# Optimization experiments

Measured on AMD Instinct MI355X. Metric: run time of the kernel, lower is better.

Reference implementation:

```python
import jax, jax.numpy as jnp
import numpy as np

N_NODES = 100000
N_EDGES = 600000
D = 128
N_CLASSES = 16


def _degrees(idx, n):
    ones = jnp.ones(idx.shape[0], dtype=jnp.float32)
    return jax.ops.segment_sum(ones, idx, num_segments=n)


def graph_conv(src, dst, h, W, b):
    # DGL GraphConv, norm='both': D_out^{-1/2} A D_in^{-1/2} h W + b
    n = h.shape[0]
    deg_out = jnp.maximum(_degrees(src, n), 1.0)
    deg_in = jnp.maximum(_degrees(dst, n), 1.0)
    h = h * jax.lax.rsqrt(deg_out)[:, None]          # src-side norm
    h = h @ W                                         # dense transform
    msg = h[src]                                      # gather  [E, d]
    agg = jax.ops.segment_sum(msg, dst, num_segments=n)  # scatter-add
    agg = agg * jax.lax.rsqrt(deg_in)[:, None]        # dst-side norm
    return agg + b


def setup_inputs() -> dict:
    key = jax.random.key(0)
    ks = jax.random.split(key, 8)
    h = jax.random.normal(ks[0], (N_NODES, D), dtype=jnp.float32)
    src = jax.random.randint(ks[1], (N_EDGES,), 0, N_NODES)
    dst = jax.random.randint(ks[2], (N_EDGES,), 0, N_NODES)
    s = 1.0 / np.sqrt(D)
    W1 = jax.random.normal(ks[3], (D, D), dtype=jnp.float32) * s
    b1 = jnp.zeros((D,), dtype=jnp.float32)
    W2 = jax.random.normal(ks[4], (D, D), dtype=jnp.float32) * s
    b2 = jnp.zeros((D,), dtype=jnp.float32)
    Wc = jax.random.normal(ks[5], (D, N_CLASSES), dtype=jnp.float32) * s
    bc = jnp.zeros((N_CLASSES,), dtype=jnp.float32)
    return {"h": h, "src": src, "dst": dst, "W1": W1, "b1": b1,
            "W2": W2, "b2": b2, "Wc": Wc, "bc": bc}


def reference(h, src, dst, W1, b1, W2, b2, Wc, bc):
    h = jax.nn.relu(graph_conv(src, dst, h, W1, b1))
    h = jax.nn.relu(graph_conv(src, dst, h, W2, b2))
    return h @ Wc + bc
```

## Files before the change

### kernel.cpp

```cpp
#include <hip/hip_runtime.h>


typedef __attribute__((ext_vector_type(4))) _Float16 half4_t;
typedef __attribute__((ext_vector_type(16))) float floatx16;

__global__ __launch_bounds__(256) void scan1_kernel(
    const int* __restrict__ cntI, const int* __restrict__ cntO,
    int* __restrict__ excl, int* __restrict__ bsum,
    float* __restrict__ rs_out, float* __restrict__ rs_in, int n)
{
    __shared__ int tmp[256];
    int i = blockIdx.x * 256 + threadIdx.x;
    int v = 0;
    if (i < n) {
        v = cntI[i];
        rs_in[i]  = rsqrtf(fmaxf((float)v, 1.0f));
        rs_out[i] = rsqrtf(fmaxf((float)cntO[i], 1.0f));
    }
    tmp[threadIdx.x] = v;
    __syncthreads();
    for (int off = 1; off < 256; off <<= 1) {
        int t = (threadIdx.x >= off) ? tmp[threadIdx.x - off] : 0;
        __syncthreads();
        tmp[threadIdx.x] += t;
        __syncthreads();
    }
    if (i < n) excl[i] = tmp[threadIdx.x] - v;
    if (threadIdx.x == 255) bsum[blockIdx.x] = tmp[255];
}

__global__ __launch_bounds__(1024) void scan2_kernel(int* __restrict__ bsum, int nb)
{
    __shared__ int tmp[1024];
    int t = threadIdx.x;
    int v = (t < nb) ? bsum[t] : 0;
    tmp[t] = v;
    __syncthreads();
    for (int off = 1; off < 1024; off <<= 1) {
        int x = (t >= off) ? tmp[t - off] : 0;
        __syncthreads();
        tmp[t] += x;
        __syncthreads();
    }
    if (t < nb) bsum[t] = tmp[t] - v;
}

__global__ __launch_bounds__(256) void scan3_kernel(
    int* __restrict__ excl, const int* __restrict__ bsum, int n)
{
    int i = blockIdx.x * 256 + threadIdx.x;
    if (i < n) excl[i] += bsum[blockIdx.x];
}

__global__ __launch_bounds__(256) void fill_kernel(
    const int* __restrict__ src, const int* __restrict__ dst,
    const int* __restrict__ rank, const int* __restrict__ starts,
    int* __restrict__ eidx, int E)
{
    int e = blockIdx.x * blockDim.x + threadIdx.x;
    if (e < E) {
        eidx[starts[dst[e]] + rank[e]] = src[e];
    }
}

__global__ __launch_bounds__(256) void wpack_kernel(
    const float* __restrict__ W1, const float* __restrict__ W2,
    _Float16* __restrict__ WB1, _Float16* __restrict__ WB2)
{
    int gid = blockIdx.x * 256 + threadIdx.x;
    int j = gid & 16383;
    int i   = j & 3;
    int col = (j >> 2) & 127;
    int g   = (j >> 9) & 1;
    int kt  = j >> 10;
    int k = kt * 8 + g * 4 + i;
    if (gid < 16384) WB1[j] = (_Float16)W1[k * 128 + col];
    else             WB2[j] = (_Float16)W2[k * 128 + col];
}

template <int MODE>
__device__ __forceinline__ void gemm_tile64(
    int bid, const void* __restrict__ Xv, const _Float16* __restrict__ WB,
    _Float16* __restrict__ T, int n)
{
    __shared__ _Float16 xa[64 * 128];
    char* xab = (char*)xa;

    const int tid  = threadIdx.x;
    const int lane = tid & 63;
    const int wv   = tid >> 6;
    const int m    = lane & 31;
    const int g    = lane >> 5;
    const int rhalf = wv & 1;
    const int chalf = wv >> 1;
    const int rbase = bid * 64 + rhalf * 32;

    {
        const int C = (tid & 31) * 4;
        const int rsub = tid >> 5;
#pragma unroll
        for (int p = 0; p < 8; ++p) {
            int R = p * 8 + rsub;
            int row = bid * 64 + R;
            half4_t a;
            if (row < n) {
                if (MODE == 0) {
                    const float* X = (const float*)Xv;
                    float4 v = *(const float4*)&X[(size_t)row * 128 + C];
                    a[0] = (_Float16)v.x;
                    a[1] = (_Float16)v.y;
                    a[2] = (_Float16)v.z;
                    a[3] = (_Float16)v.w;
                } else {
                    const _Float16* X = (const _Float16*)Xv;
                    a = *(const half4_t*)&X[(size_t)row * 128 + C];
                }
            } else {
                a[0] = a[1] = a[2] = a[3] = (_Float16)0.f;
            }
            int byte = (R * 256 + C * 2) ^ ((R & 7) << 4);
            *(half4_t*)(xab + byte) = a;
        }
    }
    __syncthreads();

    floatx16 acc0 = {}, acc1 = {};
    const int arow = rhalf * 32 + m;
    const _Float16* wb = WB + (size_t)(g * 128 + chalf * 64 + m) * 4;

#pragma unroll 2
    for (int kt = 0; kt < 16; ++kt) {
        int cbyte = kt * 16 + g * 8;
        half4_t a = *(const half4_t*)(xab + ((arow * 256 + cbyte) ^ ((m & 7) << 4)));
        const _Float16* wk = wb + (size_t)kt * 1024;
        half4_t b0 = *(const half4_t*)(wk);
        half4_t b1 = *(const half4_t*)(wk + 128);
        acc0 = __builtin_amdgcn_mfma_f32_32x32x8f16(a, b0, acc0, 0, 0, 0);
        acc1 = __builtin_amdgcn_mfma_f32_32x32x8f16(a, b1, acc1, 0, 0, 0);
    }

#pragma unroll
    for (int rg = 0; rg < 16; ++rg) {
        int rd = (rg & 3) + 8 * (rg >> 2) + 4 * g;
        int orow = rbase + rd;
        if (orow < n) {
            _Float16* tp = T + (size_t)orow * 128 + chalf * 64 + m;
            tp[0]  = (_Float16)acc0[rg];
            tp[32] = (_Float16)acc1[rg];
        }
    }
}

__global__ __launch_bounds__(256) void fused1_kernel(
    const float* __restrict__ h, const _Float16* __restrict__ WB1,
    _Float16* __restrict__ T1,
    const int* __restrict__ src, const int* __restrict__ dst,
    int* __restrict__ cntO, int* __restrict__ cntI, int* __restrict__ rank,
    int n, int E, int GB, int S)
{
    int bid = blockIdx.x;
    int g = bid / S, r = bid - g * S;
    if (r == 0 && g < GB) {
        gemm_tile64<0>(g, h, WB1, T1, n);
    } else {
        int ng = g + (r ? 1 : 0);
        if (ng > GB) ng = GB;
        int cb = bid - ng;
        int t = cb * 256 + threadIdx.x;
        if (t < E) {
            atomicAdd(&cntO[src[t]], 1);
        } else if (t < 2 * E) {
            int e = t - E;
            rank[e] = atomicAdd(&cntI[dst[e]], 1);
        }
    }
}

__global__ __launch_bounds__(256) void gemm2_kernel(
    const _Float16* __restrict__ X, const _Float16* __restrict__ WB,
    _Float16* __restrict__ T, int n)
{
    gemm_tile64<1>(blockIdx.x, X, WB, T, n);
}

template <int PES>
__device__ __forceinline__ void edge_accum(
    const _Float16* __restrict__ T, const int* __restrict__ eidx,
    const float* __restrict__ rs_out, int s0, int s1, int t, float acc[4])
{
    int j = s0;
    for (; j + 7 < s1; j += 8) {
        int4 sA = *(const int4*)&eidx[j];
        int4 sB = *(const int4*)&eidx[j + 4];
        half4_t v0 = *(const half4_t*)&T[(size_t)sA.x * 128 + t * 4];
        half4_t v1 = *(const half4_t*)&T[(size_t)sA.y * 128 + t * 4];
        half4_t v2 = *(const half4_t*)&T[(size_t)sA.z * 128 + t * 4];
        half4_t v3 = *(const half4_t*)&T[(size_t)sA.w * 128 + t * 4];
        half4_t v4 = *(const half4_t*)&T[(size_t)sB.x * 128 + t * 4];
        half4_t v5 = *(const half4_t*)&T[(size_t)sB.y * 128 + t * 4];
        half4_t v6 = *(const half4_t*)&T[(size_t)sB.z * 128 + t * 4];
        half4_t v7 = *(const half4_t*)&T[(size_t)sB.w * 128 + t * 4];
        if (PES) {
            float r0 = rs_out[sA.x], r1 = rs_out[sA.y];
            float r2 = rs_out[sA.z], r3 = rs_out[sA.w];
            float r4 = rs_out[sB.x], r5 = rs_out[sB.y];
            float r6 = rs_out[sB.z], r7 = rs_out[sB.w];
#pragma unroll
            for (int i = 0; i < 4; ++i) {
                acc[i] = fmaf((float)v0[i], r0, acc[i]);
                acc[i] = fmaf((float)v1[i], r1, acc[i]);
                acc[i] = fmaf((float)v2[i], r2, acc[i]);
                acc[i] = fmaf((float)v3[i], r3, acc[i]);
                acc[i] = fmaf((float)v4[i], r4, acc[i]);
                acc[i] = fmaf((float)v5[i], r5, acc[i]);
                acc[i] = fmaf((float)v6[i], r6, acc[i]);
                acc[i] = fmaf((float)v7[i], r7, acc[i]);
            }
        } else {
#pragma unroll
            for (int i = 0; i < 4; ++i) {
                float s01 = (float)v0[i] + (float)v1[i];
                float s23 = (float)v2[i] + (float)v3[i];
                float s45 = (float)v4[i] + (float)v5[i];
                float s67 = (float)v6[i] + (float)v7[i];
                acc[i] += (s01 + s23) + (s45 + s67);
            }
        }
    }
    if (j + 3 < s1) {
        int4 sA = *(const int4*)&eidx[j];
        half4_t v0 = *(const half4_t*)&T[(size_t)sA.x * 128 + t * 4];
        half4_t v1 = *(const half4_t*)&T[(size_t)sA.y * 128 + t * 4];
        half4_t v2 = *(const half4_t*)&T[(size_t)sA.z * 128 + t * 4];
        half4_t v3 = *(const half4_t*)&T[(size_t)sA.w * 128 + t * 4];
        if (PES) {
            float r0 = rs_out[sA.x], r1 = rs_out[sA.y];
            float r2 = rs_out[sA.z], r3 = rs_out[sA.w];
#pragma unroll
            for (int i = 0; i < 4; ++i) {
                acc[i] = fmaf((float)v0[i], r0, acc[i]);
                acc[i] = fmaf((float)v1[i], r1, acc[i]);
                acc[i] = fmaf((float)v2[i], r2, acc[i]);
                acc[i] = fmaf((float)v3[i], r3, acc[i]);
            }
        } else {
#pragma unroll
            for (int i = 0; i < 4; ++i)
                acc[i] += ((float)v0[i] + (float)v1[i]) + ((float)v2[i] + (float)v3[i]);
        }
        j += 4;
    }
    for (; j < s1; ++j) {
        int sA = eidx[j];
        half4_t va = *(const half4_t*)&T[(size_t)sA * 128 + t * 4];
        float ra = PES ? rs_out[sA] : 1.0f;
#pragma unroll
        for (int i = 0; i < 4; ++i) acc[i] = fmaf((float)va[i], ra, acc[i]);
    }
}

template <int PES, int NS>
__global__ __launch_bounds__(256) void gather_f16(
    const _Float16* __restrict__ T, const int* __restrict__ eidx,
    const int* __restrict__ starts, const float* __restrict__ rs_in,
    const float* __restrict__ rs_out, const float* __restrict__ bias,
    _Float16* __restrict__ Xout, int n, int E)
{
    int wave = (blockIdx.x * 256 + threadIdx.x) >> 6;
    int lane = threadIdx.x & 63;
    int q = lane >> 5;
    int t = lane & 31;
    int node = wave * 2 + q;
    if (node >= n) return;
    int s0 = starts[node];
    int s1 = (node + 1 < n) ? starts[node + 1] : E;

    float acc[4] = {0.f, 0.f, 0.f, 0.f};
    edge_accum<PES>(T, eidx, rs_out, s0, s1, t, acc);

    float ri = rs_in[node];
    float ro = NS ? rs_out[node] : 1.0f;
    float4 bv = *(const float4*)&bias[t * 4];
    float bb[4] = {bv.x, bv.y, bv.z, bv.w};
    half4_t o;
#pragma unroll
    for (int i = 0; i < 4; ++i) {
        float x = fmaxf(fmaf(acc[i], ri, bb[i]), 0.f) * ro;
        o[i] = (_Float16)x;
    }
    *(half4_t*)&Xout[(size_t)node * 128 + t * 4] = o;
}

__global__ __launch_bounds__(256) void classifier_kernel(
    const _Float16* __restrict__ X, const float* __restrict__ Wc,
    const float* __restrict__ bout, float* __restrict__ out, int n)
{
    __shared__ float wl[128 * 16];
    __shared__ _Float16 xs[16][128];
    const int tid = threadIdx.x;
    const int row0 = blockIdx.x * 16;
#pragma unroll
    for (int i0 = 0; i0 < 2; ++i0) {
        int i = tid + i0 * 256;
        ((float4*)wl)[i] = ((const float4*)Wc)[i];
    }
    {
        int r = tid >> 4, c8 = (tid & 15) * 8;
        int row = row0 + r;
        float4 v = make_float4(0.f, 0.f, 0.f, 0.f);
        if (row < n) v = *(const float4*)&X[(size_t)row * 128 + c8];
        *(float4*)&xs[r][c8] = v;
    }
    __syncthreads();
    int c = tid & 15, r = tid >> 4;
    float acc = 0.f;
#pragma unroll 4
    for (int k = 0; k < 128; k += 2) {
        float x0 = (float)xs[r][k];
        float x1 = (float)xs[r][k + 1];
        acc = fmaf(x0, wl[k * 16 + c], acc);
        acc = fmaf(x1, wl[(k + 1) * 16 + c], acc);
    }
    int row = row0 + r;
    if (row < n) out[(size_t)row * 16 + c] = acc + bout[c];
}

extern "C" void kernel_launch(void* const* d_in, const int* in_sizes, int n_in,
                              void* d_out, int out_size, void* d_ws, size_t ws_size,
                              hipStream_t stream)
{
    const float* h   = (const float*)d_in[0];
    const int*   src = (const int*)d_in[1];
    const int*   dst = (const int*)d_in[2];
    const float* W1  = (const float*)d_in[3];
    const float* b1  = (const float*)d_in[4];
    const float* W2  = (const float*)d_in[5];
    const float* b2  = (const float*)d_in[6];
    const float* Wc  = (const float*)d_in[7];
    const float* bc  = (const float*)d_in[8];
    float* out = (float*)d_out;

    const int n = in_sizes[0] / 128;
    const int E = in_sizes[1];
    const int nb = (n + 255) / 256;

    char* ws = (char*)d_ws;
    int*   cntO    = (int*)ws;
    int*   cntI    = cntO + n;
    int*   rank    = cntI + n;
    float* rs_out  = (float*)(rank + E);
    float* rs_in   = rs_out + n;
    int*   starts  = (int*)(rs_in + n);
    int*   bsum    = starts + n;
    int*   eidx    = bsum + 1024;
    _Float16* WB1  = (_Float16*)(eidx + E);
    _Float16* WB2  = WB1 + 16384;
    size_t off = ((size_t)((char*)(WB2 + 16384) - ws) + 255) & ~(size_t)255;
    _Float16* bufA = (_Float16*)(ws + off);
    _Float16* bufB = bufA + (size_t)n * 128;

    const int CB = (2 * E + 255) / 256;
    const int GB = (n + 63) / 64;
    const int S  = (CB + GB) / GB;

    hipMemsetAsync(cntO, 0, (size_t)2 * n * sizeof(int), stream);
    wpack_kernel<<<128, 256, 0, stream>>>(W1, W2, WB1, WB2);
    fused1_kernel<<<CB + GB, 256, 0, stream>>>(h, WB1, bufA, src, dst,
                                               cntO, cntI, rank, n, E, GB, S);
    scan1_kernel<<<nb, 256, 0, stream>>>(cntI, cntO, starts, bsum, rs_out, rs_in, n);
    scan2_kernel<<<1, 1024, 0, stream>>>(bsum, nb);
    scan3_kernel<<<nb, 256, 0, stream>>>(starts, bsum, n);
    fill_kernel<<<(E + 255) / 256, 256, 0, stream>>>(src, dst, rank, starts, eidx, E);

    int ablocks = (n + 7) / 8;

    gather_f16<1, 1><<<ablocks, 256, 0, stream>>>(bufA, eidx, starts, rs_in, rs_out, b1, bufB, n, E);

    gemm2_kernel<<<GB, 256, 0, stream>>>(bufB, WB2, bufA, n);

    gather_f16<0, 0><<<ablocks, 256, 0, stream>>>(bufA, eidx, starts, rs_in, rs_out, b2, bufB, n, E);

    classifier_kernel<<<(n + 15) / 16, 256, 0, stream>>>(bufB, Wc, bc, out, n);
}
```

Measured before the change: 195.7 us.

## Fuse layer-1 gather with layer-2 GEMM and layer-2 gather with classifier

The layer-1 aggregation now writes its 64-row output tile straight into shared memory and runs the layer-2 MFMA GEMM in the same block. The layer-2 aggregation is likewise fused into the classifier kernel. This removes two launches and the global write and read of the intermediate N×128 fp16 buffers. In exchange, the gather now runs with fewer parallel node groups per block: 64 nodes per 256-thread block, with each 32-lane group handling 8 nodes one after another. That lowers memory-level parallelism in the latency-bound gather and may cost more than the saved traffic.

```diff
diff --git a/kernel.cpp b/kernel.cpp
--- a/kernel.cpp
+++ b/kernel.cpp
@@ -78,14 +78,10 @@
     else             WB2[j] = (_Float16)W2[k * 128 + col];
 }
 
-template <int MODE>
-__device__ __forceinline__ void gemm_tile64(
-    int bid, const void* __restrict__ Xv, const _Float16* __restrict__ WB,
+__device__ __forceinline__ void mfma_and_store(
+    char* xab, int bid, const _Float16* __restrict__ WB,
     _Float16* __restrict__ T, int n)
 {
-    __shared__ _Float16 xa[64 * 128];
-    char* xab = (char*)xa;
-
     const int tid  = threadIdx.x;
     const int lane = tid & 63;
     const int wv   = tid >> 6;
@@ -94,35 +90,6 @@
     const int rhalf = wv & 1;
     const int chalf = wv >> 1;
     const int rbase = bid * 64 + rhalf * 32;
-
-    {
-        const int C = (tid & 31) * 4;
-        const int rsub = tid >> 5;
-#pragma unroll
-        for (int p = 0; p < 8; ++p) {
-            int R = p * 8 + rsub;
-            int row = bid * 64 + R;
-            half4_t a;
-            if (row < n) {
-                if (MODE == 0) {
-                    const float* X = (const float*)Xv;
-                    float4 v = *(const float4*)&X[(size_t)row * 128 + C];
-                    a[0] = (_Float16)v.x;
-                    a[1] = (_Float16)v.y;
-                    a[2] = (_Float16)v.z;
-                    a[3] = (_Float16)v.w;
-                } else {
-                    const _Float16* X = (const _Float16*)Xv;
-                    a = *(const half4_t*)&X[(size_t)row * 128 + C];
-                }
-            } else {
-                a[0] = a[1] = a[2] = a[3] = (_Float16)0.f;
-            }
-            int byte = (R * 256 + C * 2) ^ ((R & 7) << 4);
-            *(half4_t*)(xab + byte) = a;
-        }
-    }
-    __syncthreads();
 
     floatx16 acc0 = {}, acc1 = {};
     const int arow = rhalf * 32 + m;
@@ -151,6 +118,38 @@
     }
 }
 
+__device__ __forceinline__ void gemm_tile64_f32in(
+    int bid, const float* __restrict__ X, const _Float16* __restrict__ WB,
+    _Float16* __restrict__ T, int n)
+{
+    __shared__ _Float16 xa[64 * 128];
+    char* xab = (char*)xa;
+    const int tid = threadIdx.x;
+    {
+        const int C = (tid & 31) * 4;
+        const int rsub = tid >> 5;
+#pragma unroll
+        for (int p = 0; p < 8; ++p) {
+            int R = p * 8 + rsub;
+            int row = bid * 64 + R;
+            half4_t a;
+            if (row < n) {
+                float4 v = *(const float4*)&X[(size_t)row * 128 + C];
+                a[0] = (_Float16)v.x;
+                a[1] = (_Float16)v.y;
+                a[2] = (_Float16)v.z;
+                a[3] = (_Float16)v.w;
+            } else {
+                a[0] = a[1] = a[2] = a[3] = (_Float16)0.f;
+            }
+            int byte = (R * 256 + C * 2) ^ ((R & 7) << 4);
+            *(half4_t*)(xab + byte) = a;
+        }
+    }
+    __syncthreads();
+    mfma_and_store(xab, bid, WB, T, n);
+}
+
 __global__ __launch_bounds__(256) void fused1_kernel(
     const float* __restrict__ h, const _Float16* __restrict__ WB1,
     _Float16* __restrict__ T1,
@@ -161,7 +160,7 @@
     int bid = blockIdx.x;
     int g = bid / S, r = bid - g * S;
     if (r == 0 && g < GB) {
-        gemm_tile64<0>(g, h, WB1, T1, n);
+        gemm_tile64_f32in(g, h, WB1, T1, n);
     } else {
         int ng = g + (r ? 1 : 0);
         if (ng > GB) ng = GB;
@@ -174,13 +173,6 @@
             rank[e] = atomicAdd(&cntI[dst[e]], 1);
         }
     }
-}
-
-__global__ __launch_bounds__(256) void gemm2_kernel(
-    const _Float16* __restrict__ X, const _Float16* __restrict__ WB,
-    _Float16* __restrict__ T, int n)
-{
-    gemm_tile64<1>(blockIdx.x, X, WB, T, n);
 }
 
 template <int PES>
@@ -259,41 +251,51 @@
     }
 }
 
-template <int PES, int NS>
-__global__ __launch_bounds__(256) void gather_f16(
-    const _Float16* __restrict__ T, const int* __restrict__ eidx,
+__global__ __launch_bounds__(256) void g1g2_kernel(
+    const _Float16* __restrict__ T1, const int* __restrict__ eidx,
     const int* __restrict__ starts, const float* __restrict__ rs_in,
     const float* __restrict__ rs_out, const float* __restrict__ bias,
-    _Float16* __restrict__ Xout, int n, int E)
-{
-    int wave = (blockIdx.x * 256 + threadIdx.x) >> 6;
-    int lane = threadIdx.x & 63;
-    int q = lane >> 5;
-    int t = lane & 31;
-    int node = wave * 2 + q;
-    if (node >= n) return;
-    int s0 = starts[node];
-    int s1 = (node + 1 < n) ? starts[node + 1] : E;
-
-    float acc[4] = {0.f, 0.f, 0.f, 0.f};
-    edge_accum<PES>(T, eidx, rs_out, s0, s1, t, acc);
-
-    float ri = rs_in[node];
-    float ro = NS ? rs_out[node] : 1.0f;
-    float4 bv = *(const float4*)&bias[t * 4];
-    float bb[4] = {bv.x, bv.y, bv.z, bv.w};
-    half4_t o;
-#pragma unroll
-    for (int i = 0; i < 4; ++i) {
-        float x = fmaxf(fmaf(acc[i], ri, bb[i]), 0.f) * ro;
-        o[i] = (_Float16)x;
-    }
-    *(half4_t*)&Xout[(size_t)node * 128 + t * 4] = o;
-}
-
-__global__ __launch_bounds__(256) void classifier_kernel(
-    const _Float16* __restrict__ X, const float* __restrict__ Wc,
-    const float* __restrict__ bout, float* __restrict__ out, int n)
+    const _Float16* __restrict__ WB2, _Float16* __restrict__ T2, int n, int E)
+{
+    __shared__ _Float16 xa[64 * 128];
+    char* xab = (char*)xa;
+    const int tid = threadIdx.x;
+    const int grp = tid >> 5;
+    const int t   = tid & 31;
+    const int bid = blockIdx.x;
+
+#pragma unroll
+    for (int it = 0; it < 8; ++it) {
+        int R = grp * 8 + it;
+        int node = bid * 64 + R;
+        half4_t o;
+        if (node < n) {
+            int s0 = starts[node];
+            int s1 = (node + 1 < n) ? starts[node + 1] : E;
+            float acc[4] = {0.f, 0.f, 0.f, 0.f};
+            edge_accum<1>(T1, eidx, rs_out, s0, s1, t, acc);
+            float ri = rs_in[node];
+            float ro = rs_out[node];
+            float4 bv = *(const float4*)&bias[t * 4];
+            float bb[4] = {bv.x, bv.y, bv.z, bv.w};
+#pragma unroll
+            for (int i = 0; i < 4; ++i)
+                o[i] = (_Float16)(fmaxf(fmaf(acc[i], ri, bb[i]), 0.f) * ro);
+        } else {
+            o[0] = o[1] = o[2] = o[3] = (_Float16)0.f;
+        }
+        int byte = (R * 256 + t * 8) ^ ((R & 7) << 4);
+        *(half4_t*)(xab + byte) = o;
+    }
+    __syncthreads();
+    mfma_and_store(xab, bid, WB2, T2, n);
+}
+
+__global__ __launch_bounds__(256) void g2cls_kernel(
+    const _Float16* __restrict__ T2, const int* __restrict__ eidx,
+    const int* __restrict__ starts, const float* __restrict__ rs_in,
+    const float* __restrict__ bias, const float* __restrict__ Wc,
+    const float* __restrict__ bout, float* __restrict__ outp, int n, int E)
 {
     __shared__ float wl[128 * 16];
     __shared__ _Float16 xs[16][128];
@@ -304,14 +306,32 @@
         int i = tid + i0 * 256;
         ((float4*)wl)[i] = ((const float4*)Wc)[i];
     }
-    {
-        int r = tid >> 4, c8 = (tid & 15) * 8;
-        int row = row0 + r;
-        float4 v = make_float4(0.f, 0.f, 0.f, 0.f);
-        if (row < n) v = *(const float4*)&X[(size_t)row * 128 + c8];
-        *(float4*)&xs[r][c8] = v;
+
+    const int grp = tid >> 5;
+    const int t   = tid & 31;
+#pragma unroll
+    for (int it = 0; it < 2; ++it) {
+        int r = grp * 2 + it;
+        int node = row0 + r;
+        half4_t o;
+        if (node < n) {
+            int s0 = starts[node];
+            int s1 = (node + 1 < n) ? starts[node + 1] : E;
+            float acc[4] = {0.f, 0.f, 0.f, 0.f};
+            edge_accum<0>(T2, eidx, nullptr, s0, s1, t, acc);
+            float ri = rs_in[node];
+            float4 bv = *(const float4*)&bias[t * 4];
+            float bb[4] = {bv.x, bv.y, bv.z, bv.w};
+#pragma unroll
+            for (int i = 0; i < 4; ++i)
+                o[i] = (_Float16)fmaxf(fmaf(acc[i], ri, bb[i]), 0.f);
+        } else {
+            o[0] = o[1] = o[2] = o[3] = (_Float16)0.f;
+        }
+        *(half4_t*)&xs[r][t * 4] = o;
     }
     __syncthreads();
+
     int c = tid & 15, r = tid >> 4;
     float acc = 0.f;
 #pragma unroll 4
@@ -322,7 +342,7 @@
         acc = fmaf(x1, wl[(k + 1) * 16 + c], acc);
     }
     int row = row0 + r;
-    if (row < n) out[(size_t)row * 16 + c] = acc + bout[c];
+    if (row < n) outp[(size_t)row * 16 + c] = acc + bout[c];
 }
 
 extern "C" void kernel_launch(void* const* d_in, const int* in_sizes, int n_in,
@@ -372,13 +392,9 @@
     scan3_kernel<<<nb, 256, 0, stream>>>(starts, bsum, n);
     fill_kernel<<<(E + 255) / 256, 256, 0, stream>>>(src, dst, rank, starts, eidx, E);
 
-    int ablocks = (n + 7) / 8;
-
-    gather_f16<1, 1><<<ablocks, 256, 0, stream>>>(bufA, eidx, starts, rs_in, rs_out, b1, bufB, n, E);
-
-    gemm2_kernel<<<GB, 256, 0, stream>>>(bufB, WB2, bufA, n);
-
-    gather_f16<0, 0><<<ablocks, 256, 0, stream>>>(bufA, eidx, starts, rs_in, rs_out, b2, bufB, n, E);
-
-    classifier_kernel<<<(n + 15) / 16, 256, 0, stream>>>(bufB, Wc, bc, out, n);
-}
+    g1g2_kernel<<<GB, 256, 0, stream>>>(bufA, eidx, starts, rs_in, rs_out,
+                                        b1, WB2, bufB, n, E);
+
+    g2cls_kernel<<<(n + 15) / 16, 256, 0, stream>>>(bufB, eidx, starts, rs_in,
+                                                    b2, Wc, bc, out, n, E);
+}
```

After: 193.2 us. About the same (-1.3%).
